# Kernel tuning notes

Hardware: AMD Instinct MI355X
Metric: run time of the kernel (lower is better)

Reference implementation:

```python
import jax, jax.numpy as jnp
import numpy as np

DIM = 768
NUM_HEADS = 12
HEAD_DIM = DIM // NUM_HEADS


def setup_inputs() -> dict:
    key = jax.random.key(0)
    k1, k2, k3 = jax.random.split(key, 3)
    B, N, C = 1, 4096, DIM
    x = jax.random.normal(k1, (B, N, C), dtype=jnp.float32)
    w_qkv = jax.random.normal(k2, (C, 3 * C), dtype=jnp.float32) * (C ** -0.5)
    w_proj = jax.random.normal(k3, (C, C), dtype=jnp.float32) * (C ** -0.5)
    b_proj = jnp.zeros((C,), dtype=jnp.float32)
    return {"x": x, "w_qkv": w_qkv, "w_proj": w_proj, "b_proj": b_proj}


def reference(x, w_qkv, w_proj, b_proj):
    B, N, C = x.shape
    H, D = NUM_HEADS, HEAD_DIM
    scale = D ** -0.5
    # QKV projection (no bias), split into heads: [B, N, 3, H, D] -> bhnd
    qkv = (x @ w_qkv).reshape(B, N, 3, H, D)
    qkv = jnp.transpose(qkv, (2, 0, 3, 1, 4))  # [3, B, H, N, D]
    q, k, v = qkv[0], qkv[1], qkv[2]
    # world_size == 1 => all_gather is identity; full attention over N
    attn = jnp.einsum('bhnd,bhmd->bhnm', q * scale, k)
    attn = jax.nn.softmax(attn, axis=-1)
    out = jnp.einsum('bhnm,bhmd->bhnd', attn, v)
    out = jnp.transpose(out, (0, 2, 1, 3)).reshape(B, N, C)
    return out @ w_proj + b_proj
```

## Files before the change

kernel.cpp:

```cpp
#include <hip/hip_runtime.h>
#include <hip/hip_bf16.h>

#define NT 4096
#define CD 768
#define NH 12
#define HD 64
#define CQ 2304

typedef __bf16 bf;
typedef __bf16 v8bf __attribute__((ext_vector_type(8)));
typedef __bf16 v4bf __attribute__((ext_vector_type(4)));
typedef float  v4f  __attribute__((ext_vector_type(4)));

__device__ __forceinline__ void gld16(const bf* g, bf* l) {
  __builtin_amdgcn_global_load_lds(
      (__attribute__((address_space(1))) void*)g,
      (__attribute__((address_space(3))) void*)l,
      16, 0, 0);
}

__device__ __forceinline__ float fexp2(float x) {
#if defined(__HIP_DEVICE_COMPILE__)
  return __builtin_amdgcn_exp2f(x);
#else
  return x;
#endif
}

__global__ __launch_bounds__(256) void prep(
    const float* __restrict__ x, const float* __restrict__ wqkv,
    const float* __restrict__ wproj, bf* __restrict__ Xb,
    bf* __restrict__ WqkvT, bf* __restrict__ WpT) {
  __shared__ float tile[32][33];
  const int b = blockIdx.x, tid = threadIdx.x;
  if (b < 3072) {
    const int i = b * 256 + tid;
    const float4 v = ((const float4*)x)[i];
    bf o4[4] = {(bf)v.x, (bf)v.y, (bf)v.z, (bf)v.w};
    ((ushort4*)Xb)[i] = *(const ushort4*)o4;
    return;
  }
  const float* in;
  bf* out;
  int rows, cols, c0, r0;
  if (b < 4800) {
    const int t = b - 3072;
    in = wqkv; out = WqkvT; rows = CD; cols = CQ;
    c0 = (t % 72) * 32; r0 = (t / 72) * 32;
  } else {
    const int t = b - 4800;
    in = wproj; out = WpT; rows = CD; cols = CD;
    c0 = (t % 24) * 32; r0 = (t / 24) * 32;
  }
  const int tx = tid & 31, ty = tid >> 5;
#pragma unroll
  for (int j = 0; j < 32; j += 8)
    tile[ty + j][tx] = in[(size_t)(r0 + ty + j) * cols + (c0 + tx)];
  __syncthreads();
#pragma unroll
  for (int j = 0; j < 32; j += 8)
    out[(size_t)(c0 + ty + j) * rows + (r0 + tx)] = (bf)tile[tx][ty + j];
}

__global__ __launch_bounds__(256, 3) void gemm_qkv(
    const bf* __restrict__ A, const bf* __restrict__ Bt,
    bf* __restrict__ Qb, bf* __restrict__ Kb, bf* __restrict__ Vtb) {
  __shared__ __align__(16) bf As[2][128 * 32];
  __shared__ __align__(16) bf Bs[2][128 * 32];
  const int tid = threadIdx.x;
  const int lane = tid & 63, wave = tid >> 6;
  const int lane15 = lane & 15, quad = lane >> 4;
  const int waveM = wave & 1, waveN = wave >> 1;
  const int bm = blockIdx.x * 128;
  const int bn = blockIdx.y * 128;

  v4f acc[4][4];
#pragma unroll
  for (int i = 0; i < 4; ++i)
#pragma unroll
    for (int j = 0; j < 4; ++j) acc[i][j] = (v4f){0.f, 0.f, 0.f, 0.f};

  auto stageG = [&](int half, int k0) {
#pragma unroll
    for (int p = 0; p < 2; ++p) {
      const int t = tid + p * 256;
      const int r = t >> 2, c = (t & 3) * 8;
      gld16(A + (size_t)(bm + r) * CD + k0 + c, As[half] + t * 8);
    }
#pragma unroll
    for (int p = 0; p < 2; ++p) {
      const int t = tid + p * 256;
      const int r = t >> 2, c = (t & 3) * 8;
      gld16(Bt + (size_t)(bn + r) * CD + k0 + c, Bs[half] + t * 8);
    }
  };

  stageG(0, 0);
  asm volatile("s_waitcnt vmcnt(0)" ::: "memory");
  __syncthreads();

  for (int it = 0; it < CD / 32; ++it) {
    const int half = it & 1;
    if (it + 1 < CD / 32) stageG(half ^ 1, (it + 1) * 32);

    v8bf af[4], bfr[4];
#pragma unroll
    for (int mt = 0; mt < 4; ++mt)
      af[mt] = *(const v8bf*)(As[half] + (waveM * 64 + mt * 16 + lane15) * 32 + quad * 8);
#pragma unroll
    for (int nt = 0; nt < 4; ++nt)
      bfr[nt] = *(const v8bf*)(Bs[half] + (waveN * 64 + nt * 16 + lane15) * 32 + quad * 8);
#pragma unroll
    for (int mt = 0; mt < 4; ++mt)
#pragma unroll
      for (int nt = 0; nt < 4; ++nt)
        acc[mt][nt] = __builtin_amdgcn_mfma_f32_16x16x32_bf16(af[mt], bfr[nt], acc[mt][nt], 0, 0, 0);

    asm volatile("s_waitcnt vmcnt(0)" ::: "memory");
    __syncthreads();
  }

  const float QSCALE = 0.125f * 1.4426950408889634f;
#pragma unroll
  for (int mt = 0; mt < 4; ++mt) {
    const int rowB = bm + waveM * 64 + mt * 16 + quad * 4;
#pragma unroll
    for (int nt = 0; nt < 4; ++nt) {
      const int col = bn + waveN * 64 + nt * 16 + lane15;
      const int s = col / CD;
      const int rem = col - s * CD;
      const int h = rem >> 6, d = rem & 63;
      if (s == 2) {
        bf vp[4];
#pragma unroll
        for (int i = 0; i < 4; ++i) vp[i] = (bf)acc[mt][nt][i];
        const int pos = (rowB & ~31) + (((rowB & 15) >> 2) << 3) + (((rowB >> 4) & 1) << 2);
        *(uint2*)(Vtb + ((size_t)h * HD + d) * NT + pos) = *(const uint2*)vp;
      } else {
#pragma unroll
        for (int i = 0; i < 4; ++i) {
          const float v = acc[mt][nt][i];
          const int row = rowB + i;
          if (s == 0) Qb[((size_t)h * NT + row) * HD + d] = (bf)(v * QSCALE);
          else        Kb[((size_t)h * NT + row) * HD + d] = (bf)v;
        }
      }
    }
  }
}

__global__ __launch_bounds__(256, 2) void attn(
    const bf* __restrict__ Qb, const bf* __restrict__ Kb,
    const bf* __restrict__ Vtb, bf* __restrict__ Ob) {
  __shared__ __align__(16) char smem[65536];
  float* Red = (float*)smem;

  const int b = blockIdx.x;
  int h, qt;
  if (b < 512) { h = b & 7;        qt = b >> 3; }
  else { const int bb = b - 512; h = 8 + (bb & 3); qt = bb >> 2; }
  const int q0 = qt * 64;

  const int tid = threadIdx.x;
  const int wave = tid >> 6, lane = tid & 63;
  const int lane15 = lane & 15, quad = lane >> 4;

  const bf* Kh = Kb + (size_t)h * NT * HD;
  const bf* Vh = Vtb + (size_t)h * HD * NT;

  v8bf aQ[4][2];
#pragma unroll
  for (int sub = 0; sub < 4; ++sub) {
    const int qrow = q0 + sub * 16 + lane15;
    aQ[sub][0] = *(const v8bf*)(Qb + ((size_t)h * NT + qrow) * HD + quad * 8);
    aQ[sub][1] = *(const v8bf*)(Qb + ((size_t)h * NT + qrow) * HD + 32 + quad * 8);
  }

  v4f o[4][4];
#pragma unroll
  for (int sub = 0; sub < 4; ++sub)
#pragma unroll
    for (int dt = 0; dt < 4; ++dt) o[sub][dt] = (v4f){0.f, 0.f, 0.f, 0.f};
  float lsum[4] = {0.f, 0.f, 0.f, 0.f};

  auto stage = [&](int half, int kt) {
    bf* Kdst = (bf*)(smem + half * 32768);
    bf* Vdst = (bf*)(smem + half * 32768 + 16384);
#pragma unroll
    for (int p = 0; p < 4; ++p) {
      const int L = p * 256 + tid;
      const int r = L >> 3, u = L & 7;
      gld16(Kh + (size_t)(kt + r) * HD + ((u ^ (r & 7)) << 3), Kdst + L * 8);
    }
#pragma unroll
    for (int p = 0; p < 4; ++p) {
      const int L = p * 256 + tid;
      const int d = L >> 4, u = L & 15;
      gld16(Vh + (size_t)d * NT + kt + ((u ^ (d & 15)) << 3), Vdst + L * 8);
    }
  };

  stage(0, 0);
  asm volatile("s_waitcnt vmcnt(0)" ::: "memory");
  __syncthreads();

  for (int it = 0; it < NT / 128; ++it) {
    const int half = it & 1;
    if (it + 1 < NT / 128) stage(half ^ 1, (it + 1) * 128);

    const bf* Kbuf = (const bf*)(smem + half * 32768);
    const bf* Vbuf = (const bf*)(smem + half * 32768 + 16384);

    v4bf aPlo[4], aPhi[4];
#pragma unroll
    for (int e = 0; e < 2; ++e) {
      const int k = (wave * 2 + e) * 16 + lane15;
      const int k7 = k & 7;
      const v8bf bk0 = *(const v8bf*)(Kbuf + k * 64 + ((quad ^ k7) << 3));
      const v8bf bk1 = *(const v8bf*)(Kbuf + k * 64 + (((quad ^ 4) ^ k7) << 3));
#pragma unroll
      for (int sub = 0; sub < 4; ++sub) {
        v4f z = (v4f){0.f, 0.f, 0.f, 0.f};
        z = __builtin_amdgcn_mfma_f32_16x16x32_bf16(bk0, aQ[sub][0], z, 0, 0, 0);
        z = __builtin_amdgcn_mfma_f32_16x16x32_bf16(bk1, aQ[sub][1], z, 0, 0, 0);
        v4bf p4;
#pragma unroll
        for (int r = 0; r < 4; ++r) {
          const float p = fexp2(z[r]);
          lsum[sub] += p;
          p4[r] = (bf)p;
        }
        if (e == 0) aPlo[sub] = p4; else aPhi[sub] = p4;
      }
    }

#pragma unroll
    for (int dt = 0; dt < 4; ++dt) {
      const int d = dt * 16 + lane15;
      const v8bf bv = *(const v8bf*)(Vbuf + d * 128 + (((wave * 4 + quad) ^ lane15) << 3));
#pragma unroll
      for (int sub = 0; sub < 4; ++sub) {
        const v8bf aP8 = __builtin_shufflevector(aPlo[sub], aPhi[sub], 0, 1, 2, 3, 4, 5, 6, 7);
        o[sub][dt] = __builtin_amdgcn_mfma_f32_16x16x32_bf16(aP8, bv, o[sub][dt], 0, 0, 0);
      }
    }

    asm volatile("s_waitcnt vmcnt(0)" ::: "memory");
    __syncthreads();
  }

#pragma unroll
  for (int sub = 0; sub < 4; ++sub) {
    lsum[sub] += __shfl_xor(lsum[sub], 16, 64);
    lsum[sub] += __shfl_xor(lsum[sub], 32, 64);
  }

#pragma unroll
  for (int sp = 0; sp < 2; ++sp) {
    __syncthreads();
#pragma unroll
    for (int sl = 0; sl < 2; ++sl) {
      const int s = sp * 2 + sl;
      float* reg = Red + (wave * 2 + sl) * 1024;
#pragma unroll
      for (int dt = 0; dt < 4; ++dt)
        *(v4f*)(reg + dt * 256 + lane15 * 16 + quad * 4) = o[s][dt];
      if (quad == 0) Red[8192 + (wave * 2 + sl) * 16 + lane15] = lsum[s];
    }
    __syncthreads();
    const int wlo = sp * 2;
    if (wave == wlo || wave == wlo + 1) {
      const int sl = wave - wlo;
      const int s = sp * 2 + sl;
      float den = 0.f;
#pragma unroll
      for (int wv = 0; wv < 4; ++wv) den += Red[8192 + (wv * 2 + sl) * 16 + lane15];
      const float linv = 1.f / den;
#pragma unroll
      for (int dt = 0; dt < 4; ++dt) {
        v4f sum = (v4f){0.f, 0.f, 0.f, 0.f};
#pragma unroll
        for (int wv = 0; wv < 4; ++wv)
          sum += *(const v4f*)(Red + (wv * 2 + sl) * 1024 + dt * 256 + lane15 * 16 + quad * 4);
#pragma unroll
        for (int i = 0; i < 4; ++i) {
          const float linv_i = __shfl(linv, quad * 4 + i, 64);
          const int row = q0 + s * 16 + quad * 4 + i;
          Ob[(size_t)row * CD + h * HD + dt * 16 + lane15] = (bf)(sum[i] * linv_i);
        }
      }
    }
  }
}

__global__ __launch_bounds__(256, 3) void gemm_proj(
    const bf* __restrict__ A, const bf* __restrict__ Bt,
    const float* __restrict__ bias, float* __restrict__ out) {
  __shared__ __align__(16) bf As[2][128 * 32];
  __shared__ __align__(16) bf Bs[2][128 * 32];
  const int tid = threadIdx.x;
  const int lane = tid & 63, wave = tid >> 6;
  const int lane15 = lane & 15, quad = lane >> 4;
  const int waveM = wave & 1, waveN = wave >> 1;
  const int bm = blockIdx.x * 128;
  const int bn = blockIdx.y * 128;

  v4f acc[4][4];
#pragma unroll
  for (int i = 0; i < 4; ++i)
#pragma unroll
    for (int j = 0; j < 4; ++j) acc[i][j] = (v4f){0.f, 0.f, 0.f, 0.f};

  auto stageG = [&](int half, int k0) {
#pragma unroll
    for (int p = 0; p < 2; ++p) {
      const int t = tid + p * 256;
      const int r = t >> 2, c = (t & 3) * 8;
      gld16(A + (size_t)(bm + r) * CD + k0 + c, As[half] + t * 8);
    }
#pragma unroll
    for (int p = 0; p < 2; ++p) {
      const int t = tid + p * 256;
      const int r = t >> 2, c = (t & 3) * 8;
      gld16(Bt + (size_t)(bn + r) * CD + k0 + c, Bs[half] + t * 8);
    }
  };

  stageG(0, 0);
  asm volatile("s_waitcnt vmcnt(0)" ::: "memory");
  __syncthreads();

  for (int it = 0; it < CD / 32; ++it) {
    const int half = it & 1;
    if (it + 1 < CD / 32) stageG(half ^ 1, (it + 1) * 32);

    v8bf af[4], bfr[4];
#pragma unroll
    for (int mt = 0; mt < 4; ++mt)
      af[mt] = *(const v8bf*)(As[half] + (waveM * 64 + mt * 16 + lane15) * 32 + quad * 8);
#pragma unroll
    for (int nt = 0; nt < 4; ++nt)
      bfr[nt] = *(const v8bf*)(Bs[half] + (waveN * 64 + nt * 16 + lane15) * 32 + quad * 8);
#pragma unroll
    for (int mt = 0; mt < 4; ++mt)
#pragma unroll
      for (int nt = 0; nt < 4; ++nt)
        acc[mt][nt] = __builtin_amdgcn_mfma_f32_16x16x32_bf16(af[mt], bfr[nt], acc[mt][nt], 0, 0, 0);

    asm volatile("s_waitcnt vmcnt(0)" ::: "memory");
    __syncthreads();
  }

#pragma unroll
  for (int mt = 0; mt < 4; ++mt) {
    const int rowB = bm + waveM * 64 + mt * 16 + quad * 4;
#pragma unroll
    for (int nt = 0; nt < 4; ++nt) {
      const int col = bn + waveN * 64 + nt * 16 + lane15;
      const float bcol = bias[col];
#pragma unroll
      for (int i = 0; i < 4; ++i)
        out[(size_t)(rowB + i) * CD + col] = acc[mt][nt][i] + bcol;
    }
  }
}

extern "C" void kernel_launch(void* const* d_in, const int* in_sizes, int n_in,
                              void* d_out, int out_size, void* d_ws, size_t ws_size,
                              hipStream_t stream) {
  const float* x     = (const float*)d_in[0];
  const float* wqkv  = (const float*)d_in[1];
  const float* wproj = (const float*)d_in[2];
  const float* bproj = (const float*)d_in[3];
  float* out = (float*)d_out;

  bf* ws    = (bf*)d_ws;
  bf* Xb    = ws;  ws += (size_t)NT * CD;
  bf* WqkvT = ws;  ws += (size_t)CQ * CD;
  bf* WpT   = ws;  ws += (size_t)CD * CD;
  bf* Qb    = ws;  ws += (size_t)NH * NT * HD;
  bf* Kb    = ws;  ws += (size_t)NH * NT * HD;
  bf* Vtb   = ws;  ws += (size_t)NH * NT * HD;
  bf* Ob    = ws;  ws += (size_t)NT * CD;

  prep<<<5376, 256, 0, stream>>>(x, wqkv, wproj, Xb, WqkvT, WpT);
  gemm_qkv<<<dim3(NT / 128, CQ / 128), 256, 0, stream>>>(Xb, WqkvT, Qb, Kb, Vtb);
  attn<<<768, 256, 0, stream>>>(Qb, Kb, Vtb, Ob);
  gemm_proj<<<dim3(NT / 128, CD / 128), 256, 0, stream>>>(Ob, WpT, bproj, out);
}
```

Baseline: 177.3 us.

## Shrink attention LDS to single V buffer and retile projection GEMM to 64 rows

The attention kernel now double-buffers only K and keeps a single V buffer. This cuts shared memory from 64KB to 48KB so three blocks can fit per CU, and the prefetch schedule is reordered with finer vmcnt waits so K loads run two iterations ahead. The projection GEMM moves from 128x128 to 64x128 tiles with four waves each owning 32 columns, which doubles the grid to 384 blocks to fill more CUs. In exchange, V loads are exposed within each iteration, and the smaller GEMM tile reuses each loaded B tile less.

```diff
diff --git a/kernel.cpp b/kernel.cpp
--- a/kernel.cpp
+++ b/kernel.cpp
@@ -149,10 +149,10 @@
   }
 }
 
-__global__ __launch_bounds__(256, 2) void attn(
+__global__ __launch_bounds__(256, 3) void attn(
     const bf* __restrict__ Qb, const bf* __restrict__ Kb,
     const bf* __restrict__ Vtb, bf* __restrict__ Ob) {
-  __shared__ __align__(16) char smem[65536];
+  __shared__ __align__(16) char smem[49152];
   float* Red = (float*)smem;
 
   const int b = blockIdx.x;
@@ -183,15 +183,17 @@
     for (int dt = 0; dt < 4; ++dt) o[sub][dt] = (v4f){0.f, 0.f, 0.f, 0.f};
   float lsum[4] = {0.f, 0.f, 0.f, 0.f};
 
-  auto stage = [&](int half, int kt) {
-    bf* Kdst = (bf*)(smem + half * 32768);
-    bf* Vdst = (bf*)(smem + half * 32768 + 16384);
+  auto stageK = [&](int half, int kt) {
+    bf* Kdst = (bf*)(smem + half * 16384);
 #pragma unroll
     for (int p = 0; p < 4; ++p) {
       const int L = p * 256 + tid;
       const int r = L >> 3, u = L & 7;
       gld16(Kh + (size_t)(kt + r) * HD + ((u ^ (r & 7)) << 3), Kdst + L * 8);
     }
+  };
+  auto stageV = [&](int kt) {
+    bf* Vdst = (bf*)(smem + 32768);
 #pragma unroll
     for (int p = 0; p < 4; ++p) {
       const int L = p * 256 + tid;
@@ -200,16 +202,21 @@
     }
   };
 
-  stage(0, 0);
-  asm volatile("s_waitcnt vmcnt(0)" ::: "memory");
+  stageK(0, 0);
+  stageV(0);
+  stageK(1, 128);
+  asm volatile("s_waitcnt vmcnt(4)" ::: "memory");
   __syncthreads();
 
-  for (int it = 0; it < NT / 128; ++it) {
+  const int NIT = NT / 128;
+  for (int it = 0; it < NIT; ++it) {
     const int half = it & 1;
-    if (it + 1 < NT / 128) stage(half ^ 1, (it + 1) * 128);
-
-    const bf* Kbuf = (const bf*)(smem + half * 32768);
-    const bf* Vbuf = (const bf*)(smem + half * 32768 + 16384);
+    if (it > 0) {
+      if (it < NIT - 1) asm volatile("s_waitcnt vmcnt(8)" ::: "memory");
+      else              asm volatile("s_waitcnt vmcnt(4)" ::: "memory");
+    }
+    const bf* Kbuf = (const bf*)(smem + half * 16384);
+    const bf* Vbuf = (const bf*)(smem + 32768);
 
     v4bf aPlo[4], aPhi[4];
 #pragma unroll
@@ -234,6 +241,9 @@
       }
     }
 
+    if (it < NIT - 1) asm volatile("s_waitcnt vmcnt(4)" ::: "memory");
+    else              asm volatile("s_waitcnt vmcnt(0)" ::: "memory");
+
 #pragma unroll
     for (int dt = 0; dt < 4; ++dt) {
       const int d = dt * 16 + lane15;
@@ -245,8 +255,9 @@
       }
     }
 
-    asm volatile("s_waitcnt vmcnt(0)" ::: "memory");
-    __syncthreads();
+    __syncthreads();
+    if (it + 1 < NIT) stageV((it + 1) * 128);
+    if (it + 2 < NIT) stageK(half, (it + 2) * 128);
   }
 
 #pragma unroll
@@ -293,30 +304,27 @@
   }
 }
 
-__global__ __launch_bounds__(256, 3) void gemm_proj(
+__global__ __launch_bounds__(256, 4) void gemm_proj(
     const bf* __restrict__ A, const bf* __restrict__ Bt,
     const float* __restrict__ bias, float* __restrict__ out) {
-  __shared__ __align__(16) bf As[2][128 * 32];
+  __shared__ __align__(16) bf As[2][64 * 32];
   __shared__ __align__(16) bf Bs[2][128 * 32];
   const int tid = threadIdx.x;
   const int lane = tid & 63, wave = tid >> 6;
   const int lane15 = lane & 15, quad = lane >> 4;
-  const int waveM = wave & 1, waveN = wave >> 1;
-  const int bm = blockIdx.x * 128;
+  const int bm = blockIdx.x * 64;
   const int bn = blockIdx.y * 128;
 
-  v4f acc[4][4];
+  v4f acc[4][2];
 #pragma unroll
   for (int i = 0; i < 4; ++i)
 #pragma unroll
-    for (int j = 0; j < 4; ++j) acc[i][j] = (v4f){0.f, 0.f, 0.f, 0.f};
+    for (int j = 0; j < 2; ++j) acc[i][j] = (v4f){0.f, 0.f, 0.f, 0.f};
 
   auto stageG = [&](int half, int k0) {
-#pragma unroll
-    for (int p = 0; p < 2; ++p) {
-      const int t = tid + p * 256;
-      const int r = t >> 2, c = (t & 3) * 8;
-      gld16(A + (size_t)(bm + r) * CD + k0 + c, As[half] + t * 8);
+    {
+      const int r = tid >> 2, c = (tid & 3) * 8;
+      gld16(A + (size_t)(bm + r) * CD + k0 + c, As[half] + tid * 8);
     }
 #pragma unroll
     for (int p = 0; p < 2; ++p) {
@@ -334,17 +342,17 @@
     const int half = it & 1;
     if (it + 1 < CD / 32) stageG(half ^ 1, (it + 1) * 32);
 
-    v8bf af[4], bfr[4];
+    v8bf af[4], bfr[2];
 #pragma unroll
     for (int mt = 0; mt < 4; ++mt)
-      af[mt] = *(const v8bf*)(As[half] + (waveM * 64 + mt * 16 + lane15) * 32 + quad * 8);
-#pragma unroll
-    for (int nt = 0; nt < 4; ++nt)
-      bfr[nt] = *(const v8bf*)(Bs[half] + (waveN * 64 + nt * 16 + lane15) * 32 + quad * 8);
+      af[mt] = *(const v8bf*)(As[half] + (mt * 16 + lane15) * 32 + quad * 8);
+#pragma unroll
+    for (int nt = 0; nt < 2; ++nt)
+      bfr[nt] = *(const v8bf*)(Bs[half] + (wave * 32 + nt * 16 + lane15) * 32 + quad * 8);
 #pragma unroll
     for (int mt = 0; mt < 4; ++mt)
 #pragma unroll
-      for (int nt = 0; nt < 4; ++nt)
+      for (int nt = 0; nt < 2; ++nt)
         acc[mt][nt] = __builtin_amdgcn_mfma_f32_16x16x32_bf16(af[mt], bfr[nt], acc[mt][nt], 0, 0, 0);
 
     asm volatile("s_waitcnt vmcnt(0)" ::: "memory");
@@ -353,10 +361,10 @@
 
 #pragma unroll
   for (int mt = 0; mt < 4; ++mt) {
-    const int rowB = bm + waveM * 64 + mt * 16 + quad * 4;
-#pragma unroll
-    for (int nt = 0; nt < 4; ++nt) {
-      const int col = bn + waveN * 64 + nt * 16 + lane15;
+    const int rowB = bm + mt * 16 + quad * 4;
+#pragma unroll
+    for (int nt = 0; nt < 2; ++nt) {
+      const int col = bn + wave * 32 + nt * 16 + lane15;
       const float bcol = bias[col];
 #pragma unroll
       for (int i = 0; i < 4; ++i)
@@ -386,5 +394,5 @@
   prep<<<5376, 256, 0, stream>>>(x, wqkv, wproj, Xb, WqkvT, WpT);
   gemm_qkv<<<dim3(NT / 128, CQ / 128), 256, 0, stream>>>(Xb, WqkvT, Qb, Kb, Vtb);
   attn<<<768, 256, 0, stream>>>(Qb, Kb, Vtb, Ob);
-  gemm_proj<<<dim3(NT / 128, CD / 128), 256, 0, stream>>>(Ob, WpT, bproj, out);
-}
+  gemm_proj<<<dim3(NT / 64, CD / 128), 256, 0, stream>>>(Ob, WpT, bproj, out);
+}
```

Result: slower. 196.0 us (+10.6%).
